# Optimization experiments

Measured on AMD Instinct MI355X. Metric: run time of the kernel, lower is better.

## Reference

```python
import jax, jax.numpy as jnp
import numpy as np

NFEAT = 128
NHID = 64
NLAYER = 3
N_NODES = 50000
N_EDGES = 800000
N_GRAPHS = 512
BN_EPS = 1e-5


def _bn(x, gamma, beta):
    # BatchNorm1d in training mode: biased batch stats over the node axis.
    m = x.mean(axis=0)
    v = x.var(axis=0)
    return (x - m) * jax.lax.rsqrt(v + BN_EPS) * gamma + beta


def _pool(x, batch):
    # global_mean_pool: segment mean over graph ids.
    s = jax.ops.segment_sum(x, batch, num_segments=N_GRAPHS)
    c = jax.ops.segment_sum(jnp.ones((x.shape[0], 1), x.dtype), batch, num_segments=N_GRAPHS)
    return s / jnp.maximum(c, 1.0)


def setup_inputs() -> dict:
    key = jax.random.key(0)
    ks = jax.random.split(key, 16)
    x = jax.random.normal(ks[0], (N_NODES, NFEAT), dtype=jnp.float32)
    edge_index = jax.random.randint(ks[1], (2, N_EDGES), 0, N_NODES, dtype=jnp.int64)
    batch = jnp.sort(jax.random.randint(ks[2], (N_NODES,), 0, N_GRAPHS, dtype=jnp.int64))
    s_in = 1.0 / np.sqrt(NFEAT)
    s_h = 1.0 / np.sqrt(NHID)
    return {
        "x": x,
        "edge_index": edge_index,
        "batch": batch,
        "Wt": jax.random.uniform(ks[3], (NFEAT, NHID), jnp.float32, -s_in, s_in),
        "bt": jax.random.uniform(ks[4], (NHID,), jnp.float32, -s_in, s_in),
        "gt": jnp.ones((NHID,), jnp.float32),
        "bet": jnp.zeros((NHID,), jnp.float32),
        "W1": jax.random.uniform(ks[5], (NLAYER, NHID, NHID), jnp.float32, -s_h, s_h),
        "b1": jax.random.uniform(ks[6], (NLAYER, NHID), jnp.float32, -s_h, s_h),
        "W2": jax.random.uniform(ks[7], (NLAYER, NHID, NHID), jnp.float32, -s_h, s_h),
        "b2": jax.random.uniform(ks[8], (NLAYER, NHID), jnp.float32, -s_h, s_h),
        "g": jnp.ones((NLAYER, NHID), jnp.float32),
        "be": jnp.zeros((NLAYER, NHID), jnp.float32),
    }


def reference(x, edge_index, batch, Wt, bt, gt, bet, W1, b1, W2, b2, g, be):
    n = x.shape[0]
    src, dst = edge_index[0], edge_index[1]
    # input transform: Linear + BN
    h = _bn(x @ Wt + bt, gt, bet)
    embeds = [_pool(h, batch)]
    for l in range(NLAYER):
        # GINConv, eps=0: mlp(x_i + sum_{j->i} x_j); flow source->target
        agg = jax.ops.segment_sum(h[src], dst, num_segments=n)
        z = h + agg
        z = jax.nn.relu(z @ W1[l] + b1[l]) @ W2[l] + b2[l]
        h = jax.nn.relu(_bn(z, g[l], be[l]))
        embeds.append(_pool(h, batch))
    return jnp.stack(embeds)  # [NLAYER+1, N_GRAPHS, NHID]
```

## Files before the change

### kernel.cpp

```cpp
#include <hip/hip_runtime.h>

#define NFEAT   128
#define NHID    64
#define NLAYER  3
#define NNODES  50000
#define NEDGES  800000
#define NGRAPHS 512
#define BN_EPS  1e-5f
#define NPART   3125
#define MLPB    1563
#define CAP     64
#define PADW    68

typedef unsigned short u16;
typedef __attribute__((ext_vector_type(8))) short bf8;
typedef __attribute__((ext_vector_type(4))) float f32x4;

__device__ inline float b2f(u16 v) { return __uint_as_float(((unsigned)v) << 16); }
__device__ inline u16 f2b(float f) {
    unsigned u = __float_as_uint(f);
    return (u16)((u + 0x7FFF + ((u >> 16) & 1)) >> 16);
}
__device__ inline bf8 ldb8(const u16* p) {
    union { uint2 a[2]; bf8 v; } u;
    u.a[0] = *(const uint2*)p;
    u.a[1] = *(const uint2*)(p + 4);
    return u.v;
}
__device__ inline void add8(float* a, const uint4 v) {
    a[0] += __uint_as_float(v.x << 16);
    a[1] += __uint_as_float(v.x & 0xFFFF0000u);
    a[2] += __uint_as_float(v.y << 16);
    a[3] += __uint_as_float(v.y & 0xFFFF0000u);
    a[4] += __uint_as_float(v.z << 16);
    a[5] += __uint_as_float(v.z & 0xFFFF0000u);
    a[6] += __uint_as_float(v.w << 16);
    a[7] += __uint_as_float(v.w & 0xFFFF0000u);
}
__device__ inline void unp8(float* a, const uint4 v) {
    a[0] = __uint_as_float(v.x << 16);
    a[1] = __uint_as_float(v.x & 0xFFFF0000u);
    a[2] = __uint_as_float(v.y << 16);
    a[3] = __uint_as_float(v.y & 0xFFFF0000u);
    a[4] = __uint_as_float(v.z << 16);
    a[5] = __uint_as_float(v.z & 0xFFFF0000u);
    a[6] = __uint_as_float(v.w << 16);
    a[7] = __uint_as_float(v.w & 0xFFFF0000u);
}
__device__ inline uint2 pack4(float a, float b, float c, float d) {
    uint2 r;
    r.x = (unsigned)f2b(a) | ((unsigned)f2b(b) << 16);
    r.y = (unsigned)f2b(c) | ((unsigned)f2b(d) << 16);
    return r;
}

__global__ __launch_bounds__(256) void k_fill(const int* __restrict__ ei,
                                              int* __restrict__ deg,
                                              int* __restrict__ col) {
    int rangeId = blockIdx.x & 7, chunk = blockIdx.x >> 3;
    int lo = rangeId * (NNODES / 8), hi = lo + (NNODES / 8);
    int ebeg = chunk * (NEDGES / 256), eend = ebeg + (NEDGES / 256);
    for (int e = ebeg + threadIdx.x; e < eend; e += 256) {
        int dst = ei[NEDGES + e];
        if (dst >= lo && dst < hi) {
            int slot = atomicAdd(&deg[dst], 1);
            if (slot < CAP) col[dst * CAP + slot] = ei[e];
        }
    }
}

__global__ __launch_bounds__(256) void k_goff(const int* __restrict__ batch,
                                              int* __restrict__ gstart) {
    int gph = blockIdx.x * 256 + threadIdx.x;
    if (gph > NGRAPHS) return;
    if (gph == NGRAPHS) { gstart[NGRAPHS] = NNODES; return; }
    int lo = 0, hi = NNODES;
    while (lo < hi) {
        int mid = (lo + hi) >> 1;
        if (batch[mid] < gph) lo = mid + 1; else hi = mid;
    }
    gstart[gph] = lo;
}

__global__ __launch_bounds__(256) void k_wcvt(const float* __restrict__ W1,
                                              const float* __restrict__ W2,
                                              u16* __restrict__ wt) {
    int idx = blockIdx.x * 256 + threadIdx.x;
    if (idx >= NLAYER * NHID * NHID) return;
    int l = idx >> 12, rem = idx & 4095, n = rem >> 6, k = rem & 63;
    wt[l * 8192 + n * 64 + k]        = f2b(W1[l * 4096 + k * 64 + n]);
    wt[l * 8192 + 4096 + n * 64 + k] = f2b(W2[l * 4096 + k * 64 + n]);
}

__global__ __launch_bounds__(256) void k_gemm_in(const float* __restrict__ x,
                                                 const float* __restrict__ Wt,
                                                 const float* __restrict__ bt,
                                                 u16* __restrict__ zout,
                                                 float* __restrict__ partials) {
    __shared__ float sW[NFEAT * NHID];
    __shared__ float sx[16 * NFEAT];
    __shared__ float ps[4][128];
    int tid = threadIdx.x;
    const float4* W4 = (const float4*)Wt;
    float4* sW4 = (float4*)sW;
#pragma unroll
    for (int i = 0; i < NFEAT * NHID / 4 / 256; ++i) sW4[i * 256 + tid] = W4[i * 256 + tid];
    int base = blockIdx.x * 16;
    const float4* x4 = (const float4*)(x + (long long)base * NFEAT);
    float4* sx4 = (float4*)sx;
#pragma unroll
    for (int i = 0; i < 16 * NFEAT / 4 / 256; ++i) sx4[i * 256 + tid] = x4[i * 256 + tid];
    __syncthreads();
    int j = tid & 63, q = tid >> 6;
    float b = bt[j];
    float acc[4] = {b, b, b, b};
    for (int k = 0; k < NFEAT; ++k) {
        float wv = sW[k * NHID + j];
#pragma unroll
        for (int i = 0; i < 4; ++i) acc[i] += sx[(q * 4 + i) * NFEAT + k] * wv;
    }
    float s1 = 0.f, s2 = 0.f;
#pragma unroll
    for (int i = 0; i < 4; ++i) {
        zout[(base + q * 4 + i) * NHID + j] = f2b(acc[i]);
        s1 += acc[i];
        s2 += acc[i] * acc[i];
    }
    ps[q][j] = s1;
    ps[q][64 + j] = s2;
    __syncthreads();
    if (tid < 128)
        partials[blockIdx.x * 128 + tid] = ps[0][tid] + ps[1][tid] + ps[2][tid] + ps[3][tid];
}

__global__ __launch_bounds__(256) void k_red(const float* __restrict__ partials,
                                             float* __restrict__ stats, int np) {
    __shared__ float red[4];
    int c = blockIdx.x, t = threadIdx.x;
    float s = 0.f;
    for (int i = t; i < np; i += 256) s += partials[i * 128 + c];
#pragma unroll
    for (int off = 32; off >= 1; off >>= 1) s += __shfl_xor(s, off, 64);
    if ((t & 63) == 0) red[t >> 6] = s;
    __syncthreads();
    if (t == 0) stats[c] = red[0] + red[1] + red[2] + red[3];
}

__global__ __launch_bounds__(256) void k_bnh(const u16* __restrict__ z,
                                             const float* __restrict__ stats,
                                             const float* __restrict__ gamma,
                                             const float* __restrict__ beta,
                                             u16* __restrict__ h) {
    int idx = blockIdx.x * 256 + threadIdx.x;
    if (idx >= NNODES * NHID / 8) return;
    int j0 = (idx & 7) * 8;
    uint4 v = ((const uint4*)z)[idx];
    float o[8];
    unp8(o, v);
#pragma unroll
    for (int k = 0; k < 8; ++k) {
        int j = j0 + k;
        float m = stats[j] * (1.0f / NNODES);
        float var = stats[64 + j] * (1.0f / NNODES) - m * m;
        float sc = rsqrtf(var + BN_EPS) * gamma[j];
        o[k] = fmaxf(fmaf(o[k], sc, beta[j] - m * sc), 0.f);
    }
    uint4 w;
    uint2 p0 = pack4(o[0], o[1], o[2], o[3]);
    uint2 p1 = pack4(o[4], o[5], o[6], o[7]);
    w.x = p0.x; w.y = p0.y; w.z = p1.x; w.w = p1.y;
    ((uint4*)h)[idx] = w;
}

__global__ __launch_bounds__(256) void k_pool(const u16* __restrict__ z,
                                              const float* __restrict__ stats,
                                              const float* __restrict__ gamma,
                                              const float* __restrict__ beta,
                                              const int* __restrict__ gstart,
                                              float* __restrict__ out) {
    __shared__ float4 red[4][16];
    int gph = blockIdx.x;
    int lane = threadIdx.x & 63, w = threadIdx.x >> 6;
    int c = lane & 15, ws = lane >> 4;
    int slot = w * 4 + ws;
    int j0 = c * 4;
    float sc[4], sh[4];
#pragma unroll
    for (int k = 0; k < 4; ++k) {
        int j = j0 + k;
        float m = stats[j] * (1.0f / NNODES);
        float var = stats[64 + j] * (1.0f / NNODES) - m * m;
        sc[k] = rsqrtf(var + BN_EPS) * gamma[j];
        sh[k] = beta[j] - m * sc[k];
    }
    const ushort4* z4 = (const ushort4*)z;
    int s0 = gstart[gph], e0 = gstart[gph + 1];
    float a[4] = {0.f, 0.f, 0.f, 0.f};
    for (int r = s0 + slot; r < e0; r += 16) {
        ushort4 v = z4[r * 16 + c];
        a[0] += fmaxf(fmaf(b2f(v.x), sc[0], sh[0]), 0.f);
        a[1] += fmaxf(fmaf(b2f(v.y), sc[1], sh[1]), 0.f);
        a[2] += fmaxf(fmaf(b2f(v.z), sc[2], sh[2]), 0.f);
        a[3] += fmaxf(fmaf(b2f(v.w), sc[3], sh[3]), 0.f);
    }
#pragma unroll
    for (int k = 0; k < 4; ++k) {
        a[k] += __shfl_xor(a[k], 16, 64);
        a[k] += __shfl_xor(a[k], 32, 64);
    }
    if (lane < 16) red[w][c] = make_float4(a[0], a[1], a[2], a[3]);
    __syncthreads();
    if (threadIdx.x < 16) {
        float4 r0 = red[0][threadIdx.x], r1 = red[1][threadIdx.x];
        float4 r2 = red[2][threadIdx.x], r3 = red[3][threadIdx.x];
        float inv = 1.0f / fmaxf((float)(e0 - s0), 1.0f);
        float* o = &out[gph * NHID + threadIdx.x * 4];
        o[0] = (r0.x + r1.x + r2.x + r3.x) * inv;
        o[1] = (r0.y + r1.y + r2.y + r3.y) * inv;
        o[2] = (r0.z + r1.z + r2.z + r3.z) * inv;
        o[3] = (r0.w + r1.w + r2.w + r3.w) * inv;
    }
}

template <int AFFINE>
__global__ __launch_bounds__(256) void k_mlp(const u16* __restrict__ hin,
                                             const float* __restrict__ stats,
                                             const float* __restrict__ gamma,
                                             const float* __restrict__ beta,
                                             const int* __restrict__ batch,
                                             const int* __restrict__ deg,
                                             const int* __restrict__ col,
                                             const u16* __restrict__ w1t,
                                             const float* __restrict__ b1,
                                             const u16* __restrict__ w2t,
                                             const float* __restrict__ b2,
                                             u16* __restrict__ zout,
                                             float* __restrict__ partials,
                                             float* __restrict__ poolacc) {
    __shared__ u16 sW1t[NHID][PADW];
    __shared__ u16 sW2t[NHID][PADW];
    __shared__ u16 szb[32][PADW];
    __shared__ u16 stb[32][PADW];
    __shared__ float ps[128];
    int tid = threadIdx.x;

    {
        const uint4* s1 = (const uint4*)w1t;
        const uint4* s2 = (const uint4*)w2t;
#pragma unroll
        for (int i = 0; i < 2; ++i) {
            int idx = i * 256 + tid;
            int n = idx >> 3, ch = idx & 7;
            uint4 v1 = s1[idx], v2 = s2[idx];
            *(uint2*)&sW1t[n][ch * 8]     = make_uint2(v1.x, v1.y);
            *(uint2*)&sW1t[n][ch * 8 + 4] = make_uint2(v1.z, v1.w);
            *(uint2*)&sW2t[n][ch * 8]     = make_uint2(v2.x, v2.y);
            *(uint2*)&sW2t[n][ch * 8 + 4] = make_uint2(v2.z, v2.w);
        }
    }

    int w = tid >> 6, lane = tid & 63;
    int nd = lane >> 3, c8 = lane & 7;
    int node = w * 8 + nd;
    int base = blockIdx.x * 32;
    int r = base + node;
    bool rv = (r < NNODES);
    int rc = rv ? r : (NNODES - 1);
    const uint4* h16 = (const uint4*)hin;

    float sc[8], sh[8];
    if (AFFINE) {
#pragma unroll
        for (int k = 0; k < 8; ++k) {
            int j = c8 * 8 + k;
            float m = stats[j] * (1.0f / NNODES);
            float var = stats[64 + j] * (1.0f / NNODES) - m * m;
            sc[k] = rsqrtf(var + BN_EPS) * gamma[j];
            sh[k] = beta[j] - m * sc[k];
        }
    }

    float acc[8], acc2[8] = {0, 0, 0, 0, 0, 0, 0, 0};
    float selfh[8];
    {
        uint4 sv = h16[rc * 8 + c8];
        unp8(acc, sv);
#pragma unroll
        for (int k = 0; k < 8; ++k)
            selfh[k] = AFFINE ? fmaf(acc[k], sc[k], sh[k]) : acc[k];
    }
    int dd = rv ? min(deg[r], CAP) : 0;
    {
        const int* cp = col + rc * CAP;
        int t = 0;
        for (; t + 4 <= dd; t += 4) {
            int s0 = cp[t], s1 = cp[t + 1], s2 = cp[t + 2], s3 = cp[t + 3];
            uint4 v0 = h16[s0 * 8 + c8];
            uint4 v1 = h16[s1 * 8 + c8];
            uint4 v2 = h16[s2 * 8 + c8];
            uint4 v3 = h16[s3 * 8 + c8];
            add8(acc, v0); add8(acc2, v1); add8(acc, v2); add8(acc2, v3);
        }
        for (; t < dd; ++t) {
            uint4 v0 = h16[cp[t] * 8 + c8];
            add8(acc, v0);
        }
    }
    {
        float zv[8];
#pragma unroll
        for (int k = 0; k < 8; ++k) {
            float s = acc[k] + acc2[k];
            zv[k] = AFFINE ? fmaf(s, sc[k], (float)(1 + dd) * sh[k]) : s;
            if (!rv) zv[k] = 0.f;
        }
        *(uint2*)&szb[node][c8 * 8]     = pack4(zv[0], zv[1], zv[2], zv[3]);
        *(uint2*)&szb[node][c8 * 8 + 4] = pack4(zv[4], zv[5], zv[6], zv[7]);
    }

    {
        int r0 = base + w * 8;
        int myg = rv ? batch[r] : -1;
        int g_lo = batch[min(r0, NNODES - 1)];
        int g_hi = batch[min(r0 + 7, NNODES - 1)];
        for (int gg = g_lo; gg <= g_hi; ++gg) {
            float v[8];
#pragma unroll
            for (int k = 0; k < 8; ++k) {
                v[k] = (myg == gg) ? selfh[k] : 0.f;
                v[k] += __shfl_xor(v[k], 8, 64);
                v[k] += __shfl_xor(v[k], 16, 64);
                v[k] += __shfl_xor(v[k], 32, 64);
            }
            if (lane < 8) {
                float* p = &poolacc[gg * NHID + lane * 8];
#pragma unroll
                for (int k = 0; k < 8; ++k) atomicAdd(p + k, v[k]);
            }
        }
    }
    __syncthreads();

    int m = lane & 15, g = lane >> 4;
    int ncol = w * 16 + m;
    bool hiv = (base + 16 < NNODES);

    bf8 Al0 = ldb8(&szb[m][g * 8]);
    bf8 Al1 = ldb8(&szb[m][32 + g * 8]);
    bf8 Ah0 = ldb8(&szb[16 + m][g * 8]);
    bf8 Ah1 = ldb8(&szb[16 + m][32 + g * 8]);
    bf8 B0 = ldb8(&sW1t[ncol][g * 8]);
    bf8 B1 = ldb8(&sW1t[ncol][32 + g * 8]);
    float bb1 = b1[ncol];
    f32x4 cl = {bb1, bb1, bb1, bb1}, ch = {bb1, bb1, bb1, bb1};
    cl = __builtin_amdgcn_mfma_f32_16x16x32_bf16(Al0, B0, cl, 0, 0, 0);
    cl = __builtin_amdgcn_mfma_f32_16x16x32_bf16(Al1, B1, cl, 0, 0, 0);
    ch = __builtin_amdgcn_mfma_f32_16x16x32_bf16(Ah0, B0, ch, 0, 0, 0);
    ch = __builtin_amdgcn_mfma_f32_16x16x32_bf16(Ah1, B1, ch, 0, 0, 0);
#pragma unroll
    for (int i = 0; i < 4; ++i) {
        stb[g * 4 + i][ncol]      = f2b(fmaxf(cl[i], 0.f));
        stb[16 + g * 4 + i][ncol] = f2b(fmaxf(ch[i], 0.f));
    }
    __syncthreads();

    bf8 Cl0 = ldb8(&stb[m][g * 8]);
    bf8 Cl1 = ldb8(&stb[m][32 + g * 8]);
    bf8 Ch0 = ldb8(&stb[16 + m][g * 8]);
    bf8 Ch1 = ldb8(&stb[16 + m][32 + g * 8]);
    bf8 D0 = ldb8(&sW2t[ncol][g * 8]);
    bf8 D1 = ldb8(&sW2t[ncol][32 + g * 8]);
    float bb2 = b2[ncol];
    f32x4 el = {bb2, bb2, bb2, bb2}, eh = {bb2, bb2, bb2, bb2};
    el = __builtin_amdgcn_mfma_f32_16x16x32_bf16(Cl0, D0, el, 0, 0, 0);
    el = __builtin_amdgcn_mfma_f32_16x16x32_bf16(Cl1, D1, el, 0, 0, 0);
    eh = __builtin_amdgcn_mfma_f32_16x16x32_bf16(Ch0, D0, eh, 0, 0, 0);
    eh = __builtin_amdgcn_mfma_f32_16x16x32_bf16(Ch1, D1, eh, 0, 0, 0);

    float s1 = el[0] + el[1] + el[2] + el[3];
    float s2 = el[0] * el[0] + el[1] * el[1] + el[2] * el[2] + el[3] * el[3];
    if (hiv) {
        s1 += eh[0] + eh[1] + eh[2] + eh[3];
        s2 += eh[0] * eh[0] + eh[1] * eh[1] + eh[2] * eh[2] + eh[3] * eh[3];
    }
    s1 += __shfl_xor(s1, 16, 64); s1 += __shfl_xor(s1, 32, 64);
    s2 += __shfl_xor(s2, 16, 64); s2 += __shfl_xor(s2, 32, 64);
    if (lane < 16) {
        ps[w * 16 + lane] = s1;
        ps[64 + w * 16 + lane] = s2;
    }
#pragma unroll
    for (int i = 0; i < 4; ++i) {
        zout[(base + g * 4 + i) * NHID + ncol] = f2b(el[i]);
        if (hiv) zout[(base + 16 + g * 4 + i) * NHID + ncol] = f2b(eh[i]);
    }
    __syncthreads();
    if (tid < 128) partials[blockIdx.x * 128 + tid] = ps[tid];
}

__global__ __launch_bounds__(256) void k_final(const float* __restrict__ poolacc,
                                               const int* __restrict__ gstart,
                                               float* __restrict__ out) {
    int idx = blockIdx.x * 256 + threadIdx.x;
    if (idx >= NLAYER * NGRAPHS * NHID) return;
    int g = (idx >> 6) & (NGRAPHS - 1);
    float cnt = (float)(gstart[g + 1] - gstart[g]);
    out[idx] = poolacc[idx] / fmaxf(cnt, 1.0f);
}

extern "C" void kernel_launch(void* const* d_in, const int* in_sizes, int n_in,
                              void* d_out, int out_size, void* d_ws, size_t ws_size,
                              hipStream_t stream) {
    const float* x     = (const float*)d_in[0];
    const int*   ei    = (const int*)d_in[1];
    const int*   batch = (const int*)d_in[2];
    const float* Wt    = (const float*)d_in[3];
    const float* bt    = (const float*)d_in[4];
    const float* gt    = (const float*)d_in[5];
    const float* bet   = (const float*)d_in[6];
    const float* W1    = (const float*)d_in[7];
    const float* b1    = (const float*)d_in[8];
    const float* W2    = (const float*)d_in[9];
    const float* b2    = (const float*)d_in[10];
    const float* g     = (const float*)d_in[11];
    const float* be    = (const float*)d_in[12];
    float* out = (float*)d_out;

    u16* A          = (u16*)d_ws;
    u16* B          = A + NNODES * NHID;
    u16* H          = B + NNODES * NHID;
    u16* wt         = H + NNODES * NHID;
    float* partials = (float*)(wt + NLAYER * 2 * NHID * NHID);
    float* stats    = partials + NPART * 128;
    int* deg        = (int*)(stats + 4 * 128);
    float* poolacc  = (float*)(deg + NNODES);
    int* col        = (int*)(poolacc + NLAYER * NGRAPHS * NHID);
    int* gstart     = col + NNODES * CAP;

    hipMemsetAsync(deg, 0, (NNODES + NLAYER * NGRAPHS * NHID) * sizeof(int), stream);

    k_fill<<<2048, 256, 0, stream>>>(ei, deg, col);
    k_goff<<<3, 256, 0, stream>>>(batch, gstart);
    k_wcvt<<<48, 256, 0, stream>>>(W1, W2, wt);

    k_gemm_in<<<NPART, 256, 0, stream>>>(x, Wt, bt, A, partials);
    k_red<<<128, 256, 0, stream>>>(partials, stats, NPART);

    k_mlp<1><<<MLPB, 256, 0, stream>>>(A, stats, gt, bet, batch, deg, col,
                                       wt, b1, wt + 4096, b2,
                                       B, partials, poolacc);
    k_red<<<128, 256, 0, stream>>>(partials, stats + 128, MLPB);

    k_bnh<<<MLPB, 256, 0, stream>>>(B, stats + 128, g, be, H);
    k_mlp<0><<<MLPB, 256, 0, stream>>>(H, stats + 128, g, be, batch, deg, col,
                                       wt + 8192, b1 + NHID, wt + 8192 + 4096, b2 + NHID,
                                       A, partials, poolacc + NGRAPHS * NHID);
    k_red<<<128, 256, 0, stream>>>(partials, stats + 256, MLPB);

    k_bnh<<<MLPB, 256, 0, stream>>>(A, stats + 256, g + NHID, be + NHID, H);
    k_mlp<0><<<MLPB, 256, 0, stream>>>(H, stats + 256, g + NHID, be + NHID, batch, deg, col,
                                       wt + 16384, b1 + 2 * NHID, wt + 16384 + 4096, b2 + 2 * NHID,
                                       B, partials, poolacc + 2 * NGRAPHS * NHID);
    k_red<<<128, 256, 0, stream>>>(partials, stats + 384, MLPB);

    k_pool<<<NGRAPHS, 256, 0, stream>>>(B, stats + 384, g + 2 * NHID, be + 2 * NHID,
                                        gstart, out + NLAYER * NGRAPHS * NHID);
    k_final<<<(NLAYER * NGRAPHS * NHID + 255) / 256, 256, 0, stream>>>(poolacc, gstart, out);
}
```

Before: 219.3 us.

## Use bf16 MFMA for input GEMM, read MLP weights from global, widen gather unroll

The input linear layer switches from a scalar fp32 shared-memory GEMM to bf16 MFMA over 32-row tiles, with Wt pre-transposed and converted to bf16 in the weight-conversion kernel. This halves the block count and removes the 32KB fp32 weight staging in shared memory. The MLP kernels also stop copying weights into LDS and load B fragments straight from global/L2, and the neighbour gather loop is unrolled to 8 with vectorised index loads. The risks are extra bf16 rounding of x and Wt in the input projection and more global traffic for weight fragments.

After: 202.5 us. -7.7%, faster.

```diff
diff --git a/kernel.cpp b/kernel.cpp
--- a/kernel.cpp
+++ b/kernel.cpp
@@ -7,7 +7,6 @@
 #define NEDGES  800000
 #define NGRAPHS 512
 #define BN_EPS  1e-5f
-#define NPART   3125
 #define MLPB    1563
 #define CAP     64
 #define PADW    68
@@ -25,6 +24,11 @@
     union { uint2 a[2]; bf8 v; } u;
     u.a[0] = *(const uint2*)p;
     u.a[1] = *(const uint2*)(p + 4);
+    return u.v;
+}
+__device__ inline bf8 ldb8g(const u16* p) {
+    union { uint4 a; bf8 v; } u;
+    u.a = *(const uint4*)p;
     return u.v;
 }
 __device__ inline void add8(float* a, const uint4 v) {
@@ -82,55 +86,78 @@
     gstart[gph] = lo;
 }
 
-__global__ __launch_bounds__(256) void k_wcvt(const float* __restrict__ W1,
+__global__ __launch_bounds__(256) void k_wcvt(const float* __restrict__ Wt,
+                                              const float* __restrict__ W1,
                                               const float* __restrict__ W2,
+                                              u16* __restrict__ wtin,
                                               u16* __restrict__ wt) {
     int idx = blockIdx.x * 256 + threadIdx.x;
-    if (idx >= NLAYER * NHID * NHID) return;
-    int l = idx >> 12, rem = idx & 4095, n = rem >> 6, k = rem & 63;
-    wt[l * 8192 + n * 64 + k]        = f2b(W1[l * 4096 + k * 64 + n]);
-    wt[l * 8192 + 4096 + n * 64 + k] = f2b(W2[l * 4096 + k * 64 + n]);
+    if (idx < NFEAT * NHID) {
+        int n = idx >> 7, k = idx & 127;
+        wtin[n * NFEAT + k] = f2b(Wt[k * NHID + n]);
+        return;
+    }
+    idx -= NFEAT * NHID;
+    if (idx < NLAYER * NHID * NHID) {
+        int l = idx >> 12, rem = idx & 4095, n = rem >> 6, k = rem & 63;
+        wt[l * 8192 + n * 64 + k]        = f2b(W1[l * 4096 + k * 64 + n]);
+        wt[l * 8192 + 4096 + n * 64 + k] = f2b(W2[l * 4096 + k * 64 + n]);
+    }
 }
 
 __global__ __launch_bounds__(256) void k_gemm_in(const float* __restrict__ x,
-                                                 const float* __restrict__ Wt,
+                                                 const u16* __restrict__ wtin,
                                                  const float* __restrict__ bt,
                                                  u16* __restrict__ zout,
                                                  float* __restrict__ partials) {
-    __shared__ float sW[NFEAT * NHID];
-    __shared__ float sx[16 * NFEAT];
-    __shared__ float ps[4][128];
+    __shared__ u16 sx[32][132];
+    __shared__ float ps[128];
     int tid = threadIdx.x;
-    const float4* W4 = (const float4*)Wt;
-    float4* sW4 = (float4*)sW;
-#pragma unroll
-    for (int i = 0; i < NFEAT * NHID / 4 / 256; ++i) sW4[i * 256 + tid] = W4[i * 256 + tid];
-    int base = blockIdx.x * 16;
-    const float4* x4 = (const float4*)(x + (long long)base * NFEAT);
-    float4* sx4 = (float4*)sx;
-#pragma unroll
-    for (int i = 0; i < 16 * NFEAT / 4 / 256; ++i) sx4[i * 256 + tid] = x4[i * 256 + tid];
-    __syncthreads();
-    int j = tid & 63, q = tid >> 6;
-    float b = bt[j];
-    float acc[4] = {b, b, b, b};
-    for (int k = 0; k < NFEAT; ++k) {
-        float wv = sW[k * NHID + j];
-#pragma unroll
-        for (int i = 0; i < 4; ++i) acc[i] += sx[(q * 4 + i) * NFEAT + k] * wv;
-    }
-    float s1 = 0.f, s2 = 0.f;
+    int base = blockIdx.x * 32;
 #pragma unroll
     for (int i = 0; i < 4; ++i) {
-        zout[(base + q * 4 + i) * NHID + j] = f2b(acc[i]);
-        s1 += acc[i];
-        s2 += acc[i] * acc[i];
-    }
-    ps[q][j] = s1;
-    ps[q][64 + j] = s2;
-    __syncthreads();
-    if (tid < 128)
-        partials[blockIdx.x * 128 + tid] = ps[0][tid] + ps[1][tid] + ps[2][tid] + ps[3][tid];
+        int idx = i * 256 + tid;
+        int row = idx >> 5, kq = idx & 31;
+        int rc = min(base + row, NNODES - 1);
+        float4 v = ((const float4*)(x + (long long)rc * NFEAT))[kq];
+        *(uint2*)&sx[row][kq * 4] = pack4(v.x, v.y, v.z, v.w);
+    }
+    __syncthreads();
+    int w = tid >> 6, lane = tid & 63;
+    int m = lane & 15, g = lane >> 4;
+    int ncol = w * 16 + m;
+    bool hiv = (base + 16 < NNODES);
+    float bb = bt[ncol];
+    f32x4 cl = {bb, bb, bb, bb}, ch = {bb, bb, bb, bb};
+    const u16* wn = wtin + ncol * NFEAT;
+#pragma unroll
+    for (int s = 0; s < 4; ++s) {
+        int k0 = s * 32 + g * 8;
+        bf8 B  = ldb8g(wn + k0);
+        bf8 Al = ldb8(&sx[m][k0]);
+        bf8 Ah = ldb8(&sx[16 + m][k0]);
+        cl = __builtin_amdgcn_mfma_f32_16x16x32_bf16(Al, B, cl, 0, 0, 0);
+        ch = __builtin_amdgcn_mfma_f32_16x16x32_bf16(Ah, B, ch, 0, 0, 0);
+    }
+    float s1 = cl[0] + cl[1] + cl[2] + cl[3];
+    float s2 = cl[0] * cl[0] + cl[1] * cl[1] + cl[2] * cl[2] + cl[3] * cl[3];
+    if (hiv) {
+        s1 += ch[0] + ch[1] + ch[2] + ch[3];
+        s2 += ch[0] * ch[0] + ch[1] * ch[1] + ch[2] * ch[2] + ch[3] * ch[3];
+    }
+    s1 += __shfl_xor(s1, 16, 64); s1 += __shfl_xor(s1, 32, 64);
+    s2 += __shfl_xor(s2, 16, 64); s2 += __shfl_xor(s2, 32, 64);
+    if (lane < 16) {
+        ps[w * 16 + lane] = s1;
+        ps[64 + w * 16 + lane] = s2;
+    }
+#pragma unroll
+    for (int i = 0; i < 4; ++i) {
+        zout[(base + g * 4 + i) * NHID + ncol] = f2b(cl[i]);
+        if (hiv) zout[(base + 16 + g * 4 + i) * NHID + ncol] = f2b(ch[i]);
+    }
+    __syncthreads();
+    if (tid < 128) partials[blockIdx.x * 128 + tid] = ps[tid];
 }
 
 __global__ __launch_bounds__(256) void k_red(const float* __restrict__ partials,
@@ -237,28 +264,10 @@
                                              u16* __restrict__ zout,
                                              float* __restrict__ partials,
                                              float* __restrict__ poolacc) {
-    __shared__ u16 sW1t[NHID][PADW];
-    __shared__ u16 sW2t[NHID][PADW];
     __shared__ u16 szb[32][PADW];
     __shared__ u16 stb[32][PADW];
     __shared__ float ps[128];
     int tid = threadIdx.x;
-
-    {
-        const uint4* s1 = (const uint4*)w1t;
-        const uint4* s2 = (const uint4*)w2t;
-#pragma unroll
-        for (int i = 0; i < 2; ++i) {
-            int idx = i * 256 + tid;
-            int n = idx >> 3, ch = idx & 7;
-            uint4 v1 = s1[idx], v2 = s2[idx];
-            *(uint2*)&sW1t[n][ch * 8]     = make_uint2(v1.x, v1.y);
-            *(uint2*)&sW1t[n][ch * 8 + 4] = make_uint2(v1.z, v1.w);
-            *(uint2*)&sW2t[n][ch * 8]     = make_uint2(v2.x, v2.y);
-            *(uint2*)&sW2t[n][ch * 8 + 4] = make_uint2(v2.z, v2.w);
-        }
-    }
-
     int w = tid >> 6, lane = tid & 63;
     int nd = lane >> 3, c8 = lane & 7;
     int node = w * 8 + nd;
@@ -293,13 +302,28 @@
     {
         const int* cp = col + rc * CAP;
         int t = 0;
-        for (; t + 4 <= dd; t += 4) {
-            int s0 = cp[t], s1 = cp[t + 1], s2 = cp[t + 2], s3 = cp[t + 3];
-            uint4 v0 = h16[s0 * 8 + c8];
-            uint4 v1 = h16[s1 * 8 + c8];
-            uint4 v2 = h16[s2 * 8 + c8];
-            uint4 v3 = h16[s3 * 8 + c8];
+        for (; t + 8 <= dd; t += 8) {
+            int4 ia = *(const int4*)(cp + t);
+            int4 ib = *(const int4*)(cp + t + 4);
+            uint4 v0 = h16[ia.x * 8 + c8];
+            uint4 v1 = h16[ia.y * 8 + c8];
+            uint4 v2 = h16[ia.z * 8 + c8];
+            uint4 v3 = h16[ia.w * 8 + c8];
+            uint4 v4 = h16[ib.x * 8 + c8];
+            uint4 v5 = h16[ib.y * 8 + c8];
+            uint4 v6 = h16[ib.z * 8 + c8];
+            uint4 v7 = h16[ib.w * 8 + c8];
             add8(acc, v0); add8(acc2, v1); add8(acc, v2); add8(acc2, v3);
+            add8(acc, v4); add8(acc2, v5); add8(acc, v6); add8(acc2, v7);
+        }
+        if (t + 4 <= dd) {
+            int4 ia = *(const int4*)(cp + t);
+            uint4 v0 = h16[ia.x * 8 + c8];
+            uint4 v1 = h16[ia.y * 8 + c8];
+            uint4 v2 = h16[ia.z * 8 + c8];
+            uint4 v3 = h16[ia.w * 8 + c8];
+            add8(acc, v0); add8(acc2, v1); add8(acc, v2); add8(acc2, v3);
+            t += 4;
         }
         for (; t < dd; ++t) {
             uint4 v0 = h16[cp[t] * 8 + c8];
@@ -344,13 +368,15 @@
     int m = lane & 15, g = lane >> 4;
     int ncol = w * 16 + m;
     bool hiv = (base + 16 < NNODES);
+    const u16* w1n = w1t + ncol * 64;
+    const u16* w2n = w2t + ncol * 64;
 
     bf8 Al0 = ldb8(&szb[m][g * 8]);
     bf8 Al1 = ldb8(&szb[m][32 + g * 8]);
     bf8 Ah0 = ldb8(&szb[16 + m][g * 8]);
     bf8 Ah1 = ldb8(&szb[16 + m][32 + g * 8]);
-    bf8 B0 = ldb8(&sW1t[ncol][g * 8]);
-    bf8 B1 = ldb8(&sW1t[ncol][32 + g * 8]);
+    bf8 B0 = ldb8g(w1n + g * 8);
+    bf8 B1 = ldb8g(w1n + 32 + g * 8);
     float bb1 = b1[ncol];
     f32x4 cl = {bb1, bb1, bb1, bb1}, ch = {bb1, bb1, bb1, bb1};
     cl = __builtin_amdgcn_mfma_f32_16x16x32_bf16(Al0, B0, cl, 0, 0, 0);
@@ -368,8 +394,8 @@
     bf8 Cl1 = ldb8(&stb[m][32 + g * 8]);
     bf8 Ch0 = ldb8(&stb[16 + m][g * 8]);
     bf8 Ch1 = ldb8(&stb[16 + m][32 + g * 8]);
-    bf8 D0 = ldb8(&sW2t[ncol][g * 8]);
-    bf8 D1 = ldb8(&sW2t[ncol][32 + g * 8]);
+    bf8 D0 = ldb8g(w2n + g * 8);
+    bf8 D1 = ldb8g(w2n + 32 + g * 8);
     float bb2 = b2[ncol];
     f32x4 el = {bb2, bb2, bb2, bb2}, eh = {bb2, bb2, bb2, bb2};
     el = __builtin_amdgcn_mfma_f32_16x16x32_bf16(Cl0, D0, el, 0, 0, 0);
@@ -430,8 +456,9 @@
     u16* B          = A + NNODES * NHID;
     u16* H          = B + NNODES * NHID;
     u16* wt         = H + NNODES * NHID;
-    float* partials = (float*)(wt + NLAYER * 2 * NHID * NHID);
-    float* stats    = partials + NPART * 128;
+    u16* wtin       = wt + NLAYER * 2 * NHID * NHID;
+    float* partials = (float*)(wtin + NFEAT * NHID);
+    float* stats    = partials + MLPB * 128;
     int* deg        = (int*)(stats + 4 * 128);
     float* poolacc  = (float*)(deg + NNODES);
     int* col        = (int*)(poolacc + NLAYER * NGRAPHS * NHID);
@@ -441,10 +468,10 @@
 
     k_fill<<<2048, 256, 0, stream>>>(ei, deg, col);
     k_goff<<<3, 256, 0, stream>>>(batch, gstart);
-    k_wcvt<<<48, 256, 0, stream>>>(W1, W2, wt);
-
-    k_gemm_in<<<NPART, 256, 0, stream>>>(x, Wt, bt, A, partials);
-    k_red<<<128, 256, 0, stream>>>(partials, stats, NPART);
+    k_wcvt<<<80, 256, 0, stream>>>(Wt, W1, W2, wtin, wt);
+
+    k_gemm_in<<<MLPB, 256, 0, stream>>>(x, wtin, bt, A, partials);
+    k_red<<<128, 256, 0, stream>>>(partials, stats, MLPB);
 
     k_mlp<1><<<MLPB, 256, 0, stream>>>(A, stats, gt, bet, batch, deg, col,
                                        wt, b1, wt + 4096, b2,
```
